# Kernel optimization log

Measured on AMD Instinct MI355X. Metric: run time of the kernel, lower is better.

## Reference

```python
import jax, jax.numpy as jnp
import numpy as np

N = 100000          # num_nodes
E_TYPES = 5         # num_edge_type
N_EDGES = 500000    # edges per relation type
W_IN = 256
W_OUT = 128         # args.node_dim
C = 2               # args.num_channels
L = 2               # args.num_layers
NUM_CLASS = 3
BETA = 0.1


def _glorot(k, sh):
    lim = np.sqrt(6.0 / (sh[-2] + sh[-1]))
    return jax.random.uniform(k, sh, jnp.float32, -lim, lim)


def setup_inputs() -> dict:
    key = jax.random.key(0)
    ks = jax.random.split(key, 8)
    edge_index = jax.random.randint(ks[0], (E_TYPES, 2, N_EDGES), 0, N)
    edge_value = jax.random.uniform(ks[1], (E_TYPES, N_EDGES), dtype=jnp.float32)
    X = jax.random.normal(ks[2], (N, W_IN), dtype=jnp.float32)
    Ws = _glorot(ks[3], (C, W_IN, W_OUT))                      # GCNConv weights per channel
    conv_w = jax.random.normal(ks[4], (L, C, E_TYPES), dtype=jnp.float32) * 0.1  # FastGTConv weights
    lin1_w = _glorot(ks[5], (C * W_OUT, W_OUT))
    lin1_b = jnp.zeros((W_OUT,), jnp.float32)
    lin2_w = _glorot(ks[6], (W_OUT, NUM_CLASS))
    lin2_b = jnp.zeros((NUM_CLASS,), jnp.float32)
    return dict(edge_index=edge_index, edge_value=edge_value, X=X, Ws=Ws,
                conv_w=conv_w, lin1_w=lin1_w, lin1_b=lin1_b,
                lin2_w=lin2_w, lin2_b=lin2_b, num_nodes=N)


def reference(edge_index, edge_value, X, Ws, conv_w, lin1_w, lin1_b, lin2_w, lin2_b, num_nodes):
    # channel-wise input projections: X_[c] = X @ Ws[c]   -> [C, N, d]
    X_ = jnp.einsum('nf,cfo->cno', X, Ws)
    H = X_
    for l in range(L):
        filt = jax.nn.softmax(conv_w[l], axis=1)  # [C, E] per-channel softmax over edge types
        H_new = jnp.zeros_like(H)
        for j in range(E_TYPES):
            row, col = edge_index[j, 0], edge_index[j, 1]
            # sparse A_j @ H per channel: gather cols, weight by edge value, scatter-add rows
            msg = H[:, col, :] * edge_value[j][None, :, None]          # [C, Ej, d]
            agg = jax.vmap(lambda m: jax.ops.segment_sum(m, row, num_segments=num_nodes))(msg)
            H_new = H_new + filt[:, j][:, None, None] * agg
        # NOTE: source's `H = H + init_H` is Python list concat -> unused entries; no residual.
        H = H_new
    Hrelu = jax.nn.relu(BETA * X_ + (1.0 - BETA) * H)                  # [C, N, d]
    H_ = jnp.concatenate([Hrelu[c] for c in range(C)], axis=1)         # channel_agg='concat'
    H_ = H_ @ lin1_w + lin1_b                                          # [N, d]
    return H_ @ lin2_w + lin2_b                                        # [N, num_class]
```

## Files before the change

### kernel.cpp

```cpp
#include <hip/hip_runtime.h>

#define NN   100000
#define ETY  5
#define NE   500000
#define WIN  256
#define WOUT 128
#define CCH  2
#define LAY  2
#define NCLS 3

#define NTOT   (ETY * NE)
#define BSHIFT 7
#define BNODES 128
#define NBUCK  ((NN + BNODES - 1) / BNODES)
#define BCAP   4096
#define ACHUNK 8192
#define ABLK   ((NE + ACHUNK - 1) / ACHUNK)

typedef __attribute__((ext_vector_type(8))) short bf16x8;
typedef __attribute__((ext_vector_type(4))) float f32x4;

__device__ __forceinline__ unsigned short f2bf(float f) {
    union { float f; unsigned u; } v; v.f = f;
    unsigned u = v.u + 0x7FFFu + ((v.u >> 16) & 1u);
    return (unsigned short)(u >> 16);
}
__device__ __forceinline__ float bf2f(unsigned short u) {
    union { unsigned u; float f; } v; v.u = ((unsigned)u) << 16;
    return v.f;
}

__device__ __forceinline__ bf16x8 pack8(float4 a, float4 b) {
    bf16x8 r;
    r[0] = (short)f2bf(a.x); r[1] = (short)f2bf(a.y);
    r[2] = (short)f2bf(a.z); r[3] = (short)f2bf(a.w);
    r[4] = (short)f2bf(b.x); r[5] = (short)f2bf(b.y);
    r[6] = (short)f2bf(b.z); r[7] = (short)f2bf(b.w);
    return r;
}

__global__ void wconv_kernel(const float* __restrict__ Ws, const float* __restrict__ w1,
                             const float* __restrict__ conv_w,
                             unsigned short* __restrict__ Wsb, unsigned short* __restrict__ w1b,
                             float* __restrict__ filt) {
    int i = blockIdx.x * 256 + threadIdx.x;
    if (i < LAY * CCH) {
        int g = i;
        float m = -1e30f;
        for (int j = 0; j < ETY; ++j) m = fmaxf(m, conv_w[g * ETY + j]);
        float e[ETY], s = 0.f;
        for (int j = 0; j < ETY; ++j) { e[j] = __expf(conv_w[g * ETY + j] - m); s += e[j]; }
        float inv = 1.f / s;
        for (int j = 0; j < ETY; ++j) filt[g * ETY + j] = e[j] * inv;
    }
    if (i < CCH * WOUT * WIN) {
        int c = i / (WOUT * WIN);
        int r = i - c * WOUT * WIN;
        int n = r / WIN;
        int k = r - n * WIN;
        Wsb[i] = f2bf(Ws[((size_t)c * WIN + k) * WOUT + n]);
    }
    if (i < WOUT * (CCH * WOUT)) {
        int n = i / (CCH * WOUT);
        int k = i - n * (CCH * WOUT);
        w1b[i] = f2bf(w1[(size_t)k * WOUT + n]);
    }
}

__global__ void proj_kernel(const float* __restrict__ X, const unsigned short* __restrict__ Wsb,
                            unsigned short* __restrict__ Xpb) {
    const int tid  = threadIdx.x;
    const int lane = tid & 63;
    const int wv   = tid >> 6;
    const int row0 = blockIdx.x * 64 + wv * 16;
    const int ar   = lane & 15;
    const int kg   = lane >> 4;
    int arow = row0 + ar; if (arow >= NN) arow = NN - 1;
    const float* xrow = X + (size_t)arow * WIN + kg * 8;

    f32x4 acc[2][8];
#pragma unroll
    for (int c = 0; c < 2; ++c)
#pragma unroll
        for (int nt = 0; nt < 8; ++nt) acc[c][nt] = (f32x4){0.f, 0.f, 0.f, 0.f};

#pragma unroll
    for (int kk = 0; kk < 8; ++kk) {
        float4 a0 = *(const float4*)(xrow + kk * 32);
        float4 a1 = *(const float4*)(xrow + kk * 32 + 4);
        bf16x8 af = pack8(a0, a1);
#pragma unroll
        for (int c = 0; c < 2; ++c)
#pragma unroll
            for (int nt = 0; nt < 8; ++nt) {
                const bf16x8 bfm = *(const bf16x8*)(Wsb + (size_t)c * WOUT * WIN +
                                                    (size_t)(nt * 16 + ar) * WIN + kk * 32 + kg * 8);
                acc[c][nt] = __builtin_amdgcn_mfma_f32_16x16x32_bf16(af, bfm, acc[c][nt], 0, 0, 0);
            }
    }
#pragma unroll
    for (int nt = 0; nt < 8; ++nt) {
#pragma unroll
        for (int q = 0; q < 4; ++q) {
            int r = row0 + kg * 4 + q;
            if (r < NN) {
                int col = nt * 16 + ar;
                ushort2 w;
                w.x = f2bf(acc[0][nt][q]);
                w.y = f2bf(acc[1][nt][q]);
                *(ushort2*)(Xpb + (size_t)r * (WOUT * CCH) + col * 2) = w;
            }
        }
    }
}

__global__ void __launch_bounds__(256) bucket_kernel(const int* __restrict__ edge_index,
                                                     const float* __restrict__ edge_value,
                                                     int* __restrict__ bcur, int2* __restrict__ rec) {
    __shared__ int hist[NBUCK];
    __shared__ int start_s[NBUCK];
    const int tid = threadIdx.x;
    const int j = blockIdx.y;
    const int i0 = blockIdx.x * ACHUNK;
    int i1 = i0 + ACHUNK; if (i1 > NE) i1 = NE;
    const int* rows = edge_index + (size_t)j * 2 * NE;
    const int* cols = rows + NE;
    const float* evs = edge_value + (size_t)j * NE;
    for (int t = tid; t < NBUCK; t += 256) hist[t] = 0;
    __syncthreads();
    for (int i = i0 + tid; i < i1; i += 256)
        atomicAdd(&hist[rows[i] >> BSHIFT], 1);
    __syncthreads();
    for (int t = tid; t < NBUCK; t += 256) {
        int h = hist[t];
        start_s[t] = h ? atomicAdd(&bcur[t], h) : 0;
        hist[t] = 0;
    }
    __syncthreads();
    for (int i = i0 + tid; i < i1; i += 256) {
        int row = rows[i];
        int col = cols[i];
        int bk = row >> BSHIFT;
        int p = start_s[bk] + atomicAdd(&hist[bk], 1);
        if (p < BCAP)
            rec[(size_t)bk * BCAP + p] =
                make_int2(col | (j << 17) | ((row & (BNODES - 1)) << 20), __float_as_int(evs[i]));
    }
}

__global__ void __launch_bounds__(256) sortb_kernel(const int2* __restrict__ rec,
                                                    const int* __restrict__ bcur,
                                                    const float* __restrict__ filt,
                                                    int2* __restrict__ ew0F, int2* __restrict__ ew1F,
                                                    int* __restrict__ baseF, int* __restrict__ cntF) {
    __shared__ int nh[BNODES];
    __shared__ int nb[BNODES + 1];
    __shared__ int2 srec[BCAP];
    __shared__ float fl[4 * ETY];
    const int b = blockIdx.x;
    const int tid = threadIdx.x;
    int cnt = bcur[b]; if (cnt > BCAP) cnt = BCAP;
    if (tid < BNODES) nh[tid] = 0;
    if (tid < 4 * ETY) fl[tid] = filt[tid];
    __syncthreads();
    const int2* rb = rec + (size_t)b * BCAP;
    for (int k = tid; k < cnt; k += 256) {
        int r = (rb[k].x >> 20) & (BNODES - 1);
        atomicAdd(&nh[r], 1);
    }
    __syncthreads();
    if (tid < BNODES) nb[tid + 1] = nh[tid];
    if (tid == 0) nb[0] = 0;
    __syncthreads();
    for (int off = 1; off < BNODES; off <<= 1) {
        int v = 0;
        if (tid < BNODES) { v = nb[tid + 1]; if (tid + 1 > off) v += nb[tid + 1 - off]; }
        __syncthreads();
        if (tid < BNODES) nb[tid + 1] = v;
        __syncthreads();
    }
    if (tid < BNODES) nh[tid] = 0;
    __syncthreads();
    for (int k = tid; k < cnt; k += 256) {
        int2 R = rb[k];
        int r = (R.x >> 20) & (BNODES - 1);
        int p = nb[r] + atomicAdd(&nh[r], 1);
        srec[p] = R;
    }
    __syncthreads();
    const size_t g0 = (size_t)b * BCAP;
    for (int k = tid; k < cnt; k += 256) {
        int2 R = srec[k];
        int col = R.x & 0x1FFFF;
        int j = (R.x >> 17) & 7;
        float ev = __int_as_float(R.y);
        int2 E0, E1;
        E0.x = col;
        E0.y = (int)((unsigned)f2bf(fl[j] * ev) | ((unsigned)f2bf(fl[ETY + j] * ev) << 16));
        E1.x = col;
        E1.y = (int)((unsigned)f2bf(fl[2 * ETY + j] * ev) | ((unsigned)f2bf(fl[3 * ETY + j] * ev) << 16));
        ew0F[g0 + k] = E0;
        ew1F[g0 + k] = E1;
    }
    if (tid < BNODES) {
        int n = b * BNODES + tid;
        if (n < NN) {
            baseF[n] = (int)(g0 + nb[tid]);
            cntF[n]  = nb[tid + 1] - nb[tid];
        }
    }
}

__global__ void gather_kernel(const unsigned short* __restrict__ Hin, unsigned short* __restrict__ Hnew,
                              const int* __restrict__ base, const int* __restrict__ cnt,
                              const int2* __restrict__ ewF) {
    const int lane = threadIdx.x & 63;
    const int wib  = threadIdx.x >> 6;
    int n0 = blockIdx.x * 4 + wib;
    if (n0 >= NN) return;
    const int n = __builtin_amdgcn_readfirstlane(n0);
    const unsigned short* hp = Hin + lane * 4;
    float a0 = 0.f, a1 = 0.f, a2 = 0.f, a3 = 0.f;
    const int kb = __builtin_amdgcn_readfirstlane(base[n]);
    const int ce = __builtin_amdgcn_readfirstlane(cnt[n]);
    const int e = kb + ce;
    for (int k = kb; k < e; k += 8) {
        int2 es[8];
#pragma unroll
        for (int u = 0; u < 8; ++u) {
            int ku = k + u;
            es[u] = ewF[ku < e ? ku : e - 1];
        }
        ushort4 vs[8];
#pragma unroll
        for (int u = 0; u < 8; ++u)
            vs[u] = *(const ushort4*)(hp + (size_t)es[u].x * (WOUT * CCH));
#pragma unroll
        for (int u = 0; u < 8; ++u) {
            float w0 = bf2f((unsigned short)(es[u].y & 0xFFFF));
            float w1 = bf2f((unsigned short)(((unsigned)es[u].y) >> 16));
            if (k + u >= e) { w0 = 0.f; w1 = 0.f; }
            a0 = fmaf(w0, bf2f(vs[u].x), a0);
            a1 = fmaf(w1, bf2f(vs[u].y), a1);
            a2 = fmaf(w0, bf2f(vs[u].z), a2);
            a3 = fmaf(w1, bf2f(vs[u].w), a3);
        }
    }
    ushort4 r4;
    r4.x = f2bf(a0); r4.y = f2bf(a1); r4.z = f2bf(a2); r4.w = f2bf(a3);
    *(ushort4*)(Hnew + (size_t)n * (WOUT * CCH) + lane * 4) = r4;
}

__global__ void lin_kernel(const unsigned short* __restrict__ Xpb, const unsigned short* __restrict__ Hb,
                           const unsigned short* __restrict__ w1b, const float* __restrict__ b1,
                           const float* __restrict__ w2, const float* __restrict__ b2,
                           float* __restrict__ out) {
    const int tid  = threadIdx.x;
    const int lane = tid & 63;
    const int wv   = tid >> 6;
    const int row0 = blockIdx.x * 64 + wv * 16;
    const int ar   = lane & 15;
    const int kg   = lane >> 4;
    int arow = row0 + ar; if (arow >= NN) arow = NN - 1;
    const unsigned short* xr = Xpb + (size_t)arow * (WOUT * CCH);
    const unsigned short* hr = Hb  + (size_t)arow * (WOUT * CCH);

    f32x4 acc[8];
#pragma unroll
    for (int nt = 0; nt < 8; ++nt) acc[nt] = (f32x4){0.f, 0.f, 0.f, 0.f};

    bf16x8 af1s[4];
#pragma unroll
    for (int kk = 0; kk < 4; ++kk) {
        const int d = kk * 32 + kg * 8;
        bf16x8 af0, af1;
#pragma unroll
        for (int t = 0; t < 4; ++t) {
            ushort4 xu = *(const ushort4*)(xr + 2 * d + 4 * t);
            ushort4 hu = *(const ushort4*)(hr + 2 * d + 4 * t);
            float v00 = fmaxf(0.1f * bf2f(xu.x) + 0.9f * bf2f(hu.x), 0.f);
            float v01 = fmaxf(0.1f * bf2f(xu.y) + 0.9f * bf2f(hu.y), 0.f);
            float v10 = fmaxf(0.1f * bf2f(xu.z) + 0.9f * bf2f(hu.z), 0.f);
            float v11 = fmaxf(0.1f * bf2f(xu.w) + 0.9f * bf2f(hu.w), 0.f);
            af0[2 * t]     = (short)f2bf(v00);
            af0[2 * t + 1] = (short)f2bf(v10);
            af1[2 * t]     = (short)f2bf(v01);
            af1[2 * t + 1] = (short)f2bf(v11);
        }
        af1s[kk] = af1;
        const int k0 = kk * 32 + kg * 8;
#pragma unroll
        for (int nt = 0; nt < 8; ++nt) {
            const bf16x8 bfm = *(const bf16x8*)(w1b + (size_t)(nt * 16 + ar) * (CCH * WOUT) + k0);
            acc[nt] = __builtin_amdgcn_mfma_f32_16x16x32_bf16(af0, bfm, acc[nt], 0, 0, 0);
        }
    }
#pragma unroll
    for (int kk = 4; kk < 8; ++kk) {
        const int k0 = kk * 32 + kg * 8;
        const bf16x8 af = af1s[kk - 4];
#pragma unroll
        for (int nt = 0; nt < 8; ++nt) {
            const bf16x8 bfm = *(const bf16x8*)(w1b + (size_t)(nt * 16 + ar) * (CCH * WOUT) + k0);
            acc[nt] = __builtin_amdgcn_mfma_f32_16x16x32_bf16(af, bfm, acc[nt], 0, 0, 0);
        }
    }

    float b1v[8], w2v[8][NCLS];
#pragma unroll
    for (int nt = 0; nt < 8; ++nt) {
        int col = nt * 16 + ar;
        b1v[nt] = b1[col];
#pragma unroll
        for (int m = 0; m < NCLS; ++m) w2v[nt][m] = w2[col * NCLS + m];
    }
#pragma unroll
    for (int q = 0; q < 4; ++q) {
        float pm[NCLS] = {0.f, 0.f, 0.f};
#pragma unroll
        for (int nt = 0; nt < 8; ++nt) {
            float h = acc[nt][q] + b1v[nt];
#pragma unroll
            for (int m = 0; m < NCLS; ++m) pm[m] = fmaf(h, w2v[nt][m], pm[m]);
        }
#pragma unroll
        for (int m = 0; m < NCLS; ++m) {
            pm[m] += __shfl_xor(pm[m], 1);
            pm[m] += __shfl_xor(pm[m], 2);
            pm[m] += __shfl_xor(pm[m], 4);
            pm[m] += __shfl_xor(pm[m], 8);
        }
        int r = row0 + kg * 4 + q;
        if (ar == 0 && r < NN) {
            out[(size_t)r * NCLS + 0] = pm[0] + b2[0];
            out[(size_t)r * NCLS + 1] = pm[1] + b2[1];
            out[(size_t)r * NCLS + 2] = pm[2] + b2[2];
        }
    }
}

extern "C" void kernel_launch(void* const* d_in, const int* in_sizes, int n_in,
                              void* d_out, int out_size, void* d_ws, size_t ws_size,
                              hipStream_t stream) {
    const int*   edge_index = (const int*)d_in[0];
    const float* edge_value = (const float*)d_in[1];
    const float* X          = (const float*)d_in[2];
    const float* Ws         = (const float*)d_in[3];
    const float* conv_w     = (const float*)d_in[4];
    const float* lin1_w     = (const float*)d_in[5];
    const float* lin1_b     = (const float*)d_in[6];
    const float* lin2_w     = (const float*)d_in[7];
    const float* lin2_b     = (const float*)d_in[8];
    float* out = (float*)d_out;

    const size_t CNU  = (size_t)NN * WOUT * CCH;
    const size_t SLOT = (size_t)NBUCK * BCAP;
    unsigned short* Xpb = (unsigned short*)d_ws;
    unsigned short* Ab  = Xpb + CNU;
    unsigned short* Bb  = Ab + CNU;
    float*  filt  = (float*)(Bb + CNU);
    int*    bcur  = (int*)(filt + 32);
    int*    baseF = bcur + NBUCK;
    int*    cntF  = baseF + NN;
    int2*   rec   = (int2*)(cntF + NN);
    int2*   ew0F  = rec + SLOT;
    int2*   ew1F  = ew0F + SLOT;
    unsigned short* Wsb = (unsigned short*)(ew1F + SLOT);
    unsigned short* w1b = Wsb + (size_t)CCH * WOUT * WIN;

    hipMemsetAsync(bcur, 0, NBUCK * sizeof(int), stream);

    wconv_kernel<<<(CCH * WOUT * WIN + 255) / 256, 256, 0, stream>>>(Ws, lin1_w, conv_w, Wsb, w1b, filt);

    proj_kernel<<<(NN + 63) / 64, 256, 0, stream>>>(X, Wsb, Xpb);

    dim3 bg(ABLK, ETY);
    bucket_kernel<<<bg, 256, 0, stream>>>(edge_index, edge_value, bcur, rec);
    sortb_kernel<<<NBUCK, 256, 0, stream>>>(rec, bcur, filt, ew0F, ew1F, baseF, cntF);

    const int gblocks = (NN + 3) / 4;
    gather_kernel<<<gblocks, 256, 0, stream>>>(Xpb, Ab, baseF, cntF, ew0F);
    gather_kernel<<<gblocks, 256, 0, stream>>>(Ab, Bb, baseF, cntF, ew1F);

    lin_kernel<<<(NN + 63) / 64, 256, 0, stream>>>(Xpb, Bb, w1b, lin1_b, lin2_w, lin2_b, out);
}
```

Baseline: 641.6 us.

## Double proj row tile, vectorize bucket edge loads and lin input loads

```diff
diff --git a/kernel.cpp b/kernel.cpp
--- a/kernel.cpp
+++ b/kernel.cpp
@@ -18,6 +18,7 @@
 #define ABLK   ((NE + ACHUNK - 1) / ACHUNK)
 
 typedef __attribute__((ext_vector_type(8))) short bf16x8;
+typedef __attribute__((ext_vector_type(8))) unsigned short u16x8;
 typedef __attribute__((ext_vector_type(4))) float f32x4;
 
 __device__ __forceinline__ unsigned short f2bf(float f) {
@@ -67,48 +68,60 @@
     }
 }
 
-__global__ void proj_kernel(const float* __restrict__ X, const unsigned short* __restrict__ Wsb,
-                            unsigned short* __restrict__ Xpb) {
+__global__ void __launch_bounds__(256) proj_kernel(const float* __restrict__ X,
+                                                   const unsigned short* __restrict__ Wsb,
+                                                   unsigned short* __restrict__ Xpb) {
     const int tid  = threadIdx.x;
     const int lane = tid & 63;
     const int wv   = tid >> 6;
-    const int row0 = blockIdx.x * 64 + wv * 16;
+    const int row0 = blockIdx.x * 128 + wv * 32;
     const int ar   = lane & 15;
     const int kg   = lane >> 4;
-    int arow = row0 + ar; if (arow >= NN) arow = NN - 1;
-    const float* xrow = X + (size_t)arow * WIN + kg * 8;
-
-    f32x4 acc[2][8];
+    int arow0 = row0 + ar;      if (arow0 >= NN) arow0 = NN - 1;
+    int arow1 = row0 + 16 + ar; if (arow1 >= NN) arow1 = NN - 1;
+    const float* xr0 = X + (size_t)arow0 * WIN + kg * 8;
+    const float* xr1 = X + (size_t)arow1 * WIN + kg * 8;
+
+    f32x4 acc[2][2][8];
 #pragma unroll
     for (int c = 0; c < 2; ++c)
 #pragma unroll
-        for (int nt = 0; nt < 8; ++nt) acc[c][nt] = (f32x4){0.f, 0.f, 0.f, 0.f};
+        for (int rt = 0; rt < 2; ++rt)
+#pragma unroll
+            for (int nt = 0; nt < 8; ++nt) acc[c][rt][nt] = (f32x4){0.f, 0.f, 0.f, 0.f};
 
 #pragma unroll
     for (int kk = 0; kk < 8; ++kk) {
-        float4 a0 = *(const float4*)(xrow + kk * 32);
-        float4 a1 = *(const float4*)(xrow + kk * 32 + 4);
-        bf16x8 af = pack8(a0, a1);
+        float4 a00 = *(const float4*)(xr0 + kk * 32);
+        float4 a01 = *(const float4*)(xr0 + kk * 32 + 4);
+        float4 a10 = *(const float4*)(xr1 + kk * 32);
+        float4 a11 = *(const float4*)(xr1 + kk * 32 + 4);
+        bf16x8 af0 = pack8(a00, a01);
+        bf16x8 af1 = pack8(a10, a11);
 #pragma unroll
         for (int c = 0; c < 2; ++c)
 #pragma unroll
             for (int nt = 0; nt < 8; ++nt) {
                 const bf16x8 bfm = *(const bf16x8*)(Wsb + (size_t)c * WOUT * WIN +
                                                     (size_t)(nt * 16 + ar) * WIN + kk * 32 + kg * 8);
-                acc[c][nt] = __builtin_amdgcn_mfma_f32_16x16x32_bf16(af, bfm, acc[c][nt], 0, 0, 0);
+                acc[c][0][nt] = __builtin_amdgcn_mfma_f32_16x16x32_bf16(af0, bfm, acc[c][0][nt], 0, 0, 0);
+                acc[c][1][nt] = __builtin_amdgcn_mfma_f32_16x16x32_bf16(af1, bfm, acc[c][1][nt], 0, 0, 0);
             }
     }
 #pragma unroll
-    for (int nt = 0; nt < 8; ++nt) {
-#pragma unroll
-        for (int q = 0; q < 4; ++q) {
-            int r = row0 + kg * 4 + q;
-            if (r < NN) {
-                int col = nt * 16 + ar;
-                ushort2 w;
-                w.x = f2bf(acc[0][nt][q]);
-                w.y = f2bf(acc[1][nt][q]);
-                *(ushort2*)(Xpb + (size_t)r * (WOUT * CCH) + col * 2) = w;
+    for (int rt = 0; rt < 2; ++rt) {
+#pragma unroll
+        for (int nt = 0; nt < 8; ++nt) {
+#pragma unroll
+            for (int q = 0; q < 4; ++q) {
+                int r = row0 + rt * 16 + kg * 4 + q;
+                if (r < NN) {
+                    int col = nt * 16 + ar;
+                    ushort2 w;
+                    w.x = f2bf(acc[0][rt][nt][q]);
+                    w.y = f2bf(acc[1][rt][nt][q]);
+                    *(ushort2*)(Xpb + (size_t)r * (WOUT * CCH) + col * 2) = w;
+                }
             }
         }
     }
@@ -128,8 +141,13 @@
     const float* evs = edge_value + (size_t)j * NE;
     for (int t = tid; t < NBUCK; t += 256) hist[t] = 0;
     __syncthreads();
-    for (int i = i0 + tid; i < i1; i += 256)
-        atomicAdd(&hist[rows[i] >> BSHIFT], 1);
+    for (int i = i0 + tid * 4; i < i1; i += 1024) {
+        int4 r4 = *(const int4*)(rows + i);
+        atomicAdd(&hist[r4.x >> BSHIFT], 1);
+        atomicAdd(&hist[r4.y >> BSHIFT], 1);
+        atomicAdd(&hist[r4.z >> BSHIFT], 1);
+        atomicAdd(&hist[r4.w >> BSHIFT], 1);
+    }
     __syncthreads();
     for (int t = tid; t < NBUCK; t += 256) {
         int h = hist[t];
@@ -137,14 +155,21 @@
         hist[t] = 0;
     }
     __syncthreads();
-    for (int i = i0 + tid; i < i1; i += 256) {
-        int row = rows[i];
-        int col = cols[i];
-        int bk = row >> BSHIFT;
-        int p = start_s[bk] + atomicAdd(&hist[bk], 1);
-        if (p < BCAP)
-            rec[(size_t)bk * BCAP + p] =
-                make_int2(col | (j << 17) | ((row & (BNODES - 1)) << 20), __float_as_int(evs[i]));
+    for (int i = i0 + tid * 4; i < i1; i += 1024) {
+        int4 r4 = *(const int4*)(rows + i);
+        int4 c4 = *(const int4*)(cols + i);
+        float4 e4 = *(const float4*)(evs + i);
+#pragma unroll
+        for (int u = 0; u < 4; ++u) {
+            int row = (u == 0) ? r4.x : (u == 1) ? r4.y : (u == 2) ? r4.z : r4.w;
+            int col = (u == 0) ? c4.x : (u == 1) ? c4.y : (u == 2) ? c4.z : c4.w;
+            float ev = (u == 0) ? e4.x : (u == 1) ? e4.y : (u == 2) ? e4.z : e4.w;
+            int bk = row >> BSHIFT;
+            int p = start_s[bk] + atomicAdd(&hist[bk], 1);
+            if (p < BCAP)
+                rec[(size_t)bk * BCAP + p] =
+                    make_int2(col | (j << 17) | ((row & (BNODES - 1)) << 20), __float_as_int(ev));
+        }
     }
 }
 
@@ -273,19 +298,18 @@
 #pragma unroll
     for (int kk = 0; kk < 4; ++kk) {
         const int d = kk * 32 + kg * 8;
+        unsigned short xs[16], hs[16];
+        *(u16x8*)&xs[0] = *(const u16x8*)(xr + 2 * d);
+        *(u16x8*)&xs[8] = *(const u16x8*)(xr + 2 * d + 8);
+        *(u16x8*)&hs[0] = *(const u16x8*)(hr + 2 * d);
+        *(u16x8*)&hs[8] = *(const u16x8*)(hr + 2 * d + 8);
         bf16x8 af0, af1;
 #pragma unroll
-        for (int t = 0; t < 4; ++t) {
-            ushort4 xu = *(const ushort4*)(xr + 2 * d + 4 * t);
-            ushort4 hu = *(const ushort4*)(hr + 2 * d + 4 * t);
-            float v00 = fmaxf(0.1f * bf2f(xu.x) + 0.9f * bf2f(hu.x), 0.f);
-            float v01 = fmaxf(0.1f * bf2f(xu.y) + 0.9f * bf2f(hu.y), 0.f);
-            float v10 = fmaxf(0.1f * bf2f(xu.z) + 0.9f * bf2f(hu.z), 0.f);
-            float v11 = fmaxf(0.1f * bf2f(xu.w) + 0.9f * bf2f(hu.w), 0.f);
-            af0[2 * t]     = (short)f2bf(v00);
-            af0[2 * t + 1] = (short)f2bf(v10);
-            af1[2 * t]     = (short)f2bf(v01);
-            af1[2 * t + 1] = (short)f2bf(v11);
+        for (int t = 0; t < 8; ++t) {
+            float v0 = fmaxf(0.1f * bf2f(xs[2 * t])     + 0.9f * bf2f(hs[2 * t]), 0.f);
+            float v1 = fmaxf(0.1f * bf2f(xs[2 * t + 1]) + 0.9f * bf2f(hs[2 * t + 1]), 0.f);
+            af0[t] = (short)f2bf(v0);
+            af1[t] = (short)f2bf(v1);
         }
         af1s[kk] = af1;
         const int k0 = kk * 32 + kg * 8;
@@ -372,7 +396,7 @@
 
     wconv_kernel<<<(CCH * WOUT * WIN + 255) / 256, 256, 0, stream>>>(Ws, lin1_w, conv_w, Wsb, w1b, filt);
 
-    proj_kernel<<<(NN + 63) / 64, 256, 0, stream>>>(X, Wsb, Xpb);
+    proj_kernel<<<(NN + 127) / 128, 256, 0, stream>>>(X, Wsb, Xpb);
 
     dim3 bg(ABLK, ETY);
     bucket_kernel<<<bg, 256, 0, stream>>>(edge_index, edge_value, bcur, rec);
```

New measurement: 573.8 us. 1.12x faster.
